# Performance work log

Hardware: AMD Instinct MI355X
Metric: run time of the kernel (lower is better)

## Reference

```python
import jax, jax.numpy as jnp
import numpy as np

EPS = 1e-6
DIM, B, H, W = 64, 8, 256, 256

def _ln2d(x, w, b):
    # LayerNorm over channel dim per spatial location (NAFNet LayerNorm2d)
    mu = x.mean(1, keepdims=True)
    var = ((x - mu) ** 2).mean(1, keepdims=True)
    return (x - mu) * jax.lax.rsqrt(var + EPS) * w[None, :, None, None] + b[None, :, None, None]

def _pw(x, w, b):  # 1x1 conv
    return jnp.einsum('bchw,oc->bohw', x, w) + b[None, :, None, None]

def _dw(x, w, b):  # depthwise conv, SAME padding
    out = jax.lax.conv_general_dilated(x, w, (1, 1), 'SAME',
                                       feature_group_count=x.shape[1],
                                       dimension_numbers=('NCHW', 'OIHW', 'NCHW'))
    return out + b[None, :, None, None]

def _dwt(x, filt):  # haar-style non-overlapping 2x2 DWT; filt [4,2,2]
    Bn, C, Hh, Ww = x.shape
    xr = x.reshape(Bn, C, Hh // 2, 2, Ww // 2, 2)
    s = jnp.einsum('bchpwq,kpq->bkchw', xr, filt)
    return s.reshape(Bn, 4 * C, Hh // 2, Ww // 2)  # [LL..., LH..., HL..., HH...]

def _idwt(s, filt):  # inverse (transpose of orthonormal transform)
    Bn, C4, h, w = s.shape
    C = C4 // 4
    sr = s.reshape(Bn, 4, C, h, w)
    xr = jnp.einsum('bkchw,kpq->bchpwq', sr, filt)
    return xr.reshape(Bn, C, 2 * h, 2 * w)

def setup_inputs() -> dict:
    key = jax.random.key(0)
    ks = jax.random.split(key, 24)
    C = DIM
    f32 = jnp.float32
    rn = lambda k, sh, sc=0.02: (jax.random.normal(k, sh, dtype=f32) * sc)
    haar = jnp.array([[[0.5, 0.5], [0.5, 0.5]],
                      [[-0.5, -0.5], [0.5, 0.5]],
                      [[-0.5, 0.5], [-0.5, 0.5]],
                      [[0.5, -0.5], [-0.5, 0.5]]], dtype=f32)
    return {
        'x_in': jax.random.normal(ks[0], (B, C, H, W), dtype=f32),
        'filt': haar,  # learnable wavelet filters, haar-initialized
        'ln1_w': jnp.ones((C,), f32), 'ln1_b': jnp.zeros((C,), f32),
        'w1': rn(ks[1], (6 * C, 4 * C)), 'b1': rn(ks[2], (6 * C,), 0.01),
        'dw5': rn(ks[3], (6 * C, 1, 5, 5), 0.05), 'bdw5': rn(ks[4], (6 * C,), 0.01),
        'dw3': rn(ks[5], (6 * C, 1, 3, 3), 0.05), 'bdw3': rn(ks[6], (6 * C,), 0.01),
        'w2': rn(ks[7], (4 * C, 6 * C)), 'b2': rn(ks[8], (4 * C,), 0.01),
        'w_sca': rn(ks[9], (C, C)), 'b_sca': rn(ks[10], (C,), 0.01),
        'w3': rn(ks[11], (C, C)), 'b3': rn(ks[12], (C,), 0.01),
        'beta': rn(ks[13], (1, C, 1, 1), 0.1),
        'ln2_w': jnp.ones((C,), f32), 'ln2_b': jnp.zeros((C,), f32),
        'w4': rn(ks[14], (2 * C, C)), 'b4': rn(ks[15], (2 * C,), 0.01),
        'w5': rn(ks[16], (C, C)), 'b5': rn(ks[17], (C,), 0.01),
        'gamma': rn(ks[18], (1, C, 1, 1), 0.1),
    }

def reference(x_in, filt, ln1_w, ln1_b, w1, b1, dw5, bdw5, dw3, bdw3, w2, b2,
              w_sca, b_sca, w3, b3, beta, ln2_w, ln2_b, w4, b4, w5, b5, gamma):
    x = _ln2d(x_in, ln1_w, ln1_b)
    # LWN: DWT -> 1x1 expand -> depthwise(5) -> depthwise(3) -> 1x1 -> IDWT
    s = _dwt(x, filt)                  # [B,4C,H/2,W/2]
    s = _pw(s, w1, b1)                 # [B,6C,.,.]
    s = jax.nn.gelu(_dw(s, dw5, bdw5), approximate=False)
    s = jax.nn.gelu(_dw(s, dw3, bdw3), approximate=False)
    s = _pw(s, w2, b2)                 # [B,4C,.,.]
    x = _idwt(s, filt)                 # [B,C,H,W]
    # simplified channel attention (SCA)
    att = _pw(x.mean((2, 3), keepdims=True), w_sca, b_sca)
    x = x * att
    x = _pw(x, w3, b3)
    y = x_in + x * beta                # dual-residual branch 1
    x = _ln2d(y, ln2_w, ln2_b)
    x = _pw(x, w4, b4)                 # [B,2C,H,W]
    a, g = jnp.split(x, 2, axis=1)
    x = _pw(a * g, w5, b5)             # SimpleGate + project
    return y + x * gamma
```

## Files before the change

### kernel.cpp

```cpp
#include <hip/hip_runtime.h>
#include <math.h>

#define BDIM 8
#define CDIM 64
#define HDIM 256
#define WDIM 256
#define HW  (HDIM*WDIM)
#define HW2 (128*128)
#define C4  256
#define C6  384

typedef __attribute__((ext_vector_type(8))) short short8;
typedef __attribute__((ext_vector_type(4))) float f32x4;

__device__ __forceinline__ ushort f2bf(float x) {
    unsigned u = __float_as_uint(x);
    unsigned r = (u + 0x7fffu + ((u >> 16) & 1u)) >> 16;
    return (ushort)r;
}
__device__ __forceinline__ float bf2f(ushort v) {
    return __uint_as_float(((unsigned)v) << 16);
}
__device__ __forceinline__ float gelu(float x) {
    return 0.5f * x * (1.0f + erff(x * 0.70710678118654752f));
}

__global__ void k_cvt_bf16(const float* __restrict__ src, ushort* __restrict__ dst, int n) {
    int i = blockIdx.x * 256 + threadIdx.x;
    if (i < n) dst[i] = f2bf(src[i]);
}

__global__ __launch_bounds__(256) void k_ln_dwt(
    const float* __restrict__ X, const float* __restrict__ filt,
    const float* __restrict__ lw, const float* __restrict__ lb,
    ushort* __restrict__ S)
{
    const int b   = blockIdx.z;
    const int tid = threadIdx.x;
    const int pb  = tid >> 2;
    const int cg  = tid & 3;
    const int p   = blockIdx.x * 64 + pb;
    const int h2  = p >> 6;
    const int wp  = p & 63;
    float f[16];
#pragma unroll
    for (int i = 0; i < 16; ++i) f[i] = filt[i];

    const float* xb = X + (size_t)b * CDIM * HW + (size_t)(2 * h2) * WDIM + 4 * wp;
    const int c0 = cg * 16;

    float s0 = 0.f, q0 = 0.f, s1 = 0.f, q1 = 0.f;
    for (int c = c0; c < c0 + 16; ++c) {
        const float* pr = xb + (size_t)c * HW;
        float4 r0 = *(const float4*)pr;
        float4 r1 = *(const float4*)(pr + WDIM);
        s0 += r0.x + r0.y + r1.x + r1.y;
        q0 += r0.x*r0.x + r0.y*r0.y + r1.x*r1.x + r1.y*r1.y;
        s1 += r0.z + r0.w + r1.z + r1.w;
        q1 += r0.z*r0.z + r0.w*r0.w + r1.z*r1.z + r1.w*r1.w;
    }
    s0 += __shfl_xor(s0, 1); q0 += __shfl_xor(q0, 1);
    s1 += __shfl_xor(s1, 1); q1 += __shfl_xor(q1, 1);
    s0 += __shfl_xor(s0, 2); q0 += __shfl_xor(q0, 2);
    s1 += __shfl_xor(s1, 2); q1 += __shfl_xor(q1, 2);
    const float inv = 1.0f / 64.0f;
    float m0 = s0 * inv, m1 = s1 * inv;
    float rs0 = rsqrtf(fmaxf(q0 * inv - m0 * m0, 0.f) + 1e-6f);
    float rs1 = rsqrtf(fmaxf(q1 * inv - m1 * m1, 0.f) + 1e-6f);

    const int n = h2 * 128 + 2 * wp;
    ushort* Sp = S + (size_t)b * C4 * HW2;
    for (int c = c0; c < c0 + 16; ++c) {
        const float* pr = xb + (size_t)c * HW;
        float4 r0 = *(const float4*)pr;
        float4 r1 = *(const float4*)(pr + WDIM);
        float wv = lw[c], bv = lb[c];
        float a00 = (r0.x - m0) * rs0 * wv + bv;
        float a01 = (r0.y - m0) * rs0 * wv + bv;
        float a10 = (r1.x - m0) * rs0 * wv + bv;
        float a11 = (r1.y - m0) * rs0 * wv + bv;
        float b00 = (r0.z - m1) * rs1 * wv + bv;
        float b01 = (r0.w - m1) * rs1 * wv + bv;
        float b10 = (r1.z - m1) * rs1 * wv + bv;
        float b11 = (r1.w - m1) * rs1 * wv + bv;
#pragma unroll
        for (int k = 0; k < 4; ++k) {
            float va = f[k*4+0]*a00 + f[k*4+1]*a01 + f[k*4+2]*a10 + f[k*4+3]*a11;
            float vb = f[k*4+0]*b00 + f[k*4+1]*b01 + f[k*4+2]*b10 + f[k*4+3]*b11;
            unsigned pk = (unsigned)f2bf(va) | ((unsigned)f2bf(vb) << 16);
            *(unsigned*)&Sp[(size_t)(k * CDIM + c) * HW2 + n] = pk;
        }
    }
}

template<bool BF16OUT>
__global__ __launch_bounds__(256) void k_pw_mfma(
    const ushort* __restrict__ A, const float* __restrict__ bias,
    const ushort* __restrict__ Xg, void* __restrict__ Yg,
    int M, int K, int N)
{
    const int b  = blockIdx.z;
    const int m0 = blockIdx.y * 128;
    const int n0 = blockIdx.x * 128;
    const ushort* X = Xg + (size_t)b * K * N;

    __shared__ ushort As[128][72];
    __shared__ ushort Bs[128][72];

    const int tid = threadIdx.x;
    const int l   = tid & 63, w = tid >> 6;
    const int wr  = w >> 1, wc = w & 1;
    const int lr  = l & 15, lg = l >> 4;

    const int blr = tid & 15;
    const int bng = tid >> 4;
    const int k0c = blr * 4;
    const int n0t = bng * 8;

    f32x4 acc[4][4];
#pragma unroll
    for (int i = 0; i < 4; ++i)
#pragma unroll
        for (int j = 0; j < 4; ++j) acc[i][j] = (f32x4){0.f, 0.f, 0.f, 0.f};

    for (int k0 = 0; k0 < K; k0 += 64) {
        uint4 av[4], bv[4];
#pragma unroll
        for (int i = 0; i < 4; ++i) {
            int c = tid + 256 * i;
            int m = c & 127, kc = c >> 7;
            av[i] = *(const uint4*)(A + (size_t)(m0 + m) * K + k0 + kc * 8);
        }
#pragma unroll
        for (int dk = 0; dk < 4; ++dk)
            bv[dk] = *(const uint4*)(X + (size_t)(k0 + k0c + dk) * N + n0 + n0t);

        __syncthreads();
#pragma unroll
        for (int i = 0; i < 4; ++i) {
            int c = tid + 256 * i;
            int m = c & 127, kc = c >> 7;
            *(uint4*)&As[m][kc * 8] = av[i];
        }
#pragma unroll
        for (int j = 0; j < 8; ++j) {
            ushort4 wv;
            wv.x = ((const ushort*)&bv[0])[j];
            wv.y = ((const ushort*)&bv[1])[j];
            wv.z = ((const ushort*)&bv[2])[j];
            wv.w = ((const ushort*)&bv[3])[j];
            *(ushort4*)&Bs[n0t + j][k0c] = wv;
        }
        __syncthreads();

#pragma unroll
        for (int ks = 0; ks < 2; ++ks) {
            short8 af[4], bf[4];
#pragma unroll
            for (int mf = 0; mf < 4; ++mf)
                af[mf] = *(const short8*)&As[wr * 64 + mf * 16 + lr][ks * 32 + lg * 8];
#pragma unroll
            for (int nf = 0; nf < 4; ++nf)
                bf[nf] = *(const short8*)&Bs[wc * 64 + nf * 16 + lr][ks * 32 + lg * 8];
#pragma unroll
            for (int mf = 0; mf < 4; ++mf)
#pragma unroll
                for (int nf = 0; nf < 4; ++nf)
                    acc[mf][nf] = __builtin_amdgcn_mfma_f32_16x16x32_bf16(
                        af[mf], bf[nf], acc[mf][nf], 0, 0, 0);
        }
    }

#pragma unroll
    for (int mf = 0; mf < 4; ++mf) {
#pragma unroll
        for (int r = 0; r < 4; ++r) {
            int m = m0 + wr * 64 + mf * 16 + lg * 4 + r;
            float bi = bias[m];
#pragma unroll
            for (int nf = 0; nf < 4; ++nf) {
                int n = n0 + wc * 64 + nf * 16 + lr;
                float v = acc[mf][nf][r] + bi;
                if (BF16OUT)
                    ((ushort*)Yg)[(size_t)b * M * N + (size_t)m * N + n] = f2bf(v);
                else
                    ((float*)Yg)[(size_t)b * M * N + (size_t)m * N + n] = v;
            }
        }
    }
}

__global__ __launch_bounds__(256) void k_dw_fused(
    const ushort* __restrict__ X, const float* __restrict__ W5,
    const float* __restrict__ B5, const float* __restrict__ W3,
    const float* __restrict__ B3, ushort* __restrict__ Y)
{
    const int b = blockIdx.z, ch = blockIdx.y;
    const int ty0 = (blockIdx.x >> 1) * 64, tx0 = (blockIdx.x & 1) * 64;
    __shared__ ushort in_s[70][72];
    __shared__ float  mid_s[66][68];
    const ushort* Xc = X + ((size_t)b * C6 + ch) * HW2;
    ushort* Yc = Y + ((size_t)b * C6 + ch) * HW2;
    const int tid = threadIdx.x;

    float w5[25], w3[9];
#pragma unroll
    for (int i = 0; i < 25; ++i) w5[i] = W5[ch * 25 + i];
#pragma unroll
    for (int i = 0; i < 9; ++i)  w3[i] = W3[ch * 9 + i];
    const float b5v = B5[ch], b3v = B3[ch];

    for (int e = tid; e < 70 * 72; e += 256) {
        int r = e / 72, c = e - r * 72;
        int gy = ty0 + r - 3, gx = tx0 + c - 3;
        ushort v = 0;
        if (c < 70 && (unsigned)gy < 128u && (unsigned)gx < 128u)
            v = Xc[gy * 128 + gx];
        in_s[r][c] = v;
    }
    __syncthreads();

    for (int g = tid; g < 66 * 17; g += 256) {
        int r = g / 17, cg = g - r * 17;
        int c = cg * 4;
        float xin[5][8];
#pragma unroll
        for (int dr = 0; dr < 5; ++dr) {
            ushort4 lo = *(const ushort4*)&in_s[r + dr][c];
            ushort4 hi = *(const ushort4*)&in_s[r + dr][c + 4];
            xin[dr][0] = bf2f(lo.x); xin[dr][1] = bf2f(lo.y);
            xin[dr][2] = bf2f(lo.z); xin[dr][3] = bf2f(lo.w);
            xin[dr][4] = bf2f(hi.x); xin[dr][5] = bf2f(hi.y);
            xin[dr][6] = bf2f(hi.z); xin[dr][7] = bf2f(hi.w);
        }
        int gy = ty0 + r - 1;
        float o[4];
#pragma unroll
        for (int j = 0; j < 4; ++j) {
            float acc = b5v;
#pragma unroll
            for (int dr = 0; dr < 5; ++dr)
#pragma unroll
                for (int dc = 0; dc < 5; ++dc)
                    acc += xin[dr][j + dc] * w5[dr * 5 + dc];
            int gx = tx0 + c + j - 1;
            bool ok = ((unsigned)gy < 128u) && ((unsigned)gx < 128u);
            o[j] = ok ? gelu(acc) : 0.f;
        }
        *(float4*)&mid_s[r][c] = make_float4(o[0], o[1], o[2], o[3]);
    }
    __syncthreads();

    for (int g = tid; g < 64 * 16; g += 256) {
        int r = g >> 4, c = (g & 15) * 4;
        float mv[3][8];
#pragma unroll
        for (int dr = 0; dr < 3; ++dr) {
            float4 a = *(const float4*)&mid_s[r + dr][c];
            float4 bq = *(const float4*)&mid_s[r + dr][c + 4];
            mv[dr][0] = a.x; mv[dr][1] = a.y; mv[dr][2] = a.z; mv[dr][3] = a.w;
            mv[dr][4] = bq.x; mv[dr][5] = bq.y; mv[dr][6] = bq.z; mv[dr][7] = bq.w;
        }
        ushort4 ov;
        float oo[4];
#pragma unroll
        for (int j = 0; j < 4; ++j) {
            float acc = b3v;
#pragma unroll
            for (int dr = 0; dr < 3; ++dr)
#pragma unroll
                for (int dc = 0; dc < 3; ++dc)
                    acc += mv[dr][j + dc] * w3[dr * 3 + dc];
            oo[j] = gelu(acc);
        }
        ov.x = f2bf(oo[0]); ov.y = f2bf(oo[1]); ov.z = f2bf(oo[2]); ov.w = f2bf(oo[3]);
        *(ushort4*)&Yc[(ty0 + r) * 128 + tx0 + c] = ov;
    }
}

__global__ __launch_bounds__(256) void k_idwt(
    const float* __restrict__ S, const float* __restrict__ filt,
    float* __restrict__ Xw, float* __restrict__ sumbuf)
{
    const int b = blockIdx.z, c = blockIdx.y;
    const int tid = threadIdx.x;
    const int n = blockIdx.x * 256 + tid;
    const int h2 = n >> 7, w2 = n & 127;
    float f[16];
#pragma unroll
    for (int i = 0; i < 16; ++i) f[i] = filt[i];
    float sv[4];
#pragma unroll
    for (int k = 0; k < 4; ++k)
        sv[k] = S[((size_t)b * C4 + k * CDIM + c) * HW2 + n];
    float* xp = Xw + ((size_t)b * CDIM + c) * HW + (size_t)(2 * h2) * WDIM + 2 * w2;
    float local = 0.f;
#pragma unroll
    for (int p = 0; p < 2; ++p)
#pragma unroll
        for (int q = 0; q < 2; ++q) {
            float v = sv[0] * f[0*4 + p*2 + q] + sv[1] * f[1*4 + p*2 + q]
                    + sv[2] * f[2*4 + p*2 + q] + sv[3] * f[3*4 + p*2 + q];
            xp[p * WDIM + q] = v;
            local += v;
        }
    __shared__ float red[256];
    red[tid] = local;
    __syncthreads();
    for (int off = 128; off > 0; off >>= 1) {
        if (tid < off) red[tid] += red[tid + off];
        __syncthreads();
    }
    if (tid == 0) atomicAdd(&sumbuf[b * CDIM + c], red[0]);
}

__global__ void k_att(const float* __restrict__ sumbuf, const float* __restrict__ Wsca,
                      const float* __restrict__ bsca, float* __restrict__ att)
{
    int t = threadIdx.x;
    int b = t >> 6, o = t & 63;
    float acc = bsca[o];
    const float s = 1.0f / (float)HW;
    for (int c = 0; c < 64; ++c)
        acc += Wsca[o * 64 + c] * (sumbuf[b * 64 + c] * s);
    att[t] = acc;
}

__global__ __launch_bounds__(256) void k_sca_pw3(
    const float* __restrict__ Xw, const float* __restrict__ Xin,
    const float* __restrict__ att, const float* __restrict__ W3,
    const float* __restrict__ b3, const float* __restrict__ beta,
    float* __restrict__ Yb)
{
    __shared__ __align__(16) float w3s[64 * 64];
    __shared__ float atts[64], b3s[64], bets[64];
    const int tid = threadIdx.x, b = blockIdx.z;
    for (int i = tid; i < 4096; i += 256) w3s[i] = W3[i];
    if (tid < 64) { atts[tid] = att[b * 64 + tid]; b3s[tid] = b3[tid]; bets[tid] = beta[tid]; }
    __syncthreads();
    const size_t n = (size_t)blockIdx.x * 256 + tid;
    const size_t base = (size_t)b * 64 * HW + n;
    float v[64];
#pragma unroll
    for (int c = 0; c < 64; ++c) v[c] = Xw[base + (size_t)c * HW] * atts[c];
    for (int o = 0; o < 64; ++o) {
        float acc = b3s[o];
        const float4* wr = (const float4*)&w3s[o * 64];
#pragma unroll
        for (int c4 = 0; c4 < 16; ++c4) {
            float4 wv = wr[c4]; int c = c4 * 4;
            acc += wv.x*v[c] + wv.y*v[c+1] + wv.z*v[c+2] + wv.w*v[c+3];
        }
        Yb[base + (size_t)o * HW] = Xin[base + (size_t)o * HW] + acc * bets[o];
    }
}

__global__ __launch_bounds__(256) void k_ln2_pw4(
    const float* __restrict__ Yb, const float* __restrict__ lw,
    const float* __restrict__ lb, const float* __restrict__ W4,
    const float* __restrict__ b4, float* __restrict__ Hb)
{
    __shared__ __align__(16) float w4s[128 * 64];
    __shared__ float b4s[128], lws[64], lbs[64];
    const int tid = threadIdx.x, b = blockIdx.z;
    for (int i = tid; i < 8192; i += 256) w4s[i] = W4[i];
    if (tid < 128) b4s[tid] = b4[tid];
    if (tid < 64) { lws[tid] = lw[tid]; lbs[tid] = lb[tid]; }
    __syncthreads();
    const size_t n = (size_t)blockIdx.x * 256 + tid;
    const size_t base = (size_t)b * 64 * HW + n;
    float t[64]; float sum = 0.f, sq = 0.f;
#pragma unroll
    for (int c = 0; c < 64; ++c) {
        float yv = Yb[base + (size_t)c * HW];
        t[c] = yv; sum += yv; sq += yv * yv;
    }
    float mu = sum * (1.0f / 64.0f);
    float var = sq * (1.0f / 64.0f) - mu * mu;
    float rs = rsqrtf(fmaxf(var, 0.f) + 1e-6f);
#pragma unroll
    for (int c = 0; c < 64; ++c) t[c] = (t[c] - mu) * rs * lws[c] + lbs[c];
    for (int j = 0; j < 64; ++j) {
        float aj = b4s[j], gj = b4s[j + 64];
        const float4* wa = (const float4*)&w4s[j * 64];
        const float4* wg = (const float4*)&w4s[(j + 64) * 64];
#pragma unroll
        for (int c4 = 0; c4 < 16; ++c4) {
            float4 va = wa[c4], vg = wg[c4]; int c = c4 * 4;
            aj += va.x*t[c] + va.y*t[c+1] + va.z*t[c+2] + va.w*t[c+3];
            gj += vg.x*t[c] + vg.y*t[c+1] + vg.z*t[c+2] + vg.w*t[c+3];
        }
        Hb[((size_t)b * 64 + j) * HW + n] = aj * gj;
    }
}

__global__ __launch_bounds__(256) void k_pw5_out(
    const float* __restrict__ Yb, const float* __restrict__ Hb,
    const float* __restrict__ W5, const float* __restrict__ b5,
    const float* __restrict__ gamma, float* __restrict__ Out)
{
    __shared__ __align__(16) float w5s[64 * 64];
    __shared__ float b5s[64], gs[64];
    const int tid = threadIdx.x, b = blockIdx.z;
    for (int i = tid; i < 4096; i += 256) w5s[i] = W5[i];
    if (tid < 64) { b5s[tid] = b5[tid]; gs[tid] = gamma[tid]; }
    __syncthreads();
    const size_t n = (size_t)blockIdx.x * 256 + tid;
    const size_t base = (size_t)b * 64 * HW + n;
    float hv[64];
#pragma unroll
    for (int j = 0; j < 64; ++j) hv[j] = Hb[base + (size_t)j * HW];
    for (int o = 0; o < 64; ++o) {
        float acc = b5s[o];
        const float4* wr = (const float4*)&w5s[o * 64];
#pragma unroll
        for (int j4 = 0; j4 < 16; ++j4) {
            float4 wv = wr[j4]; int j = j4 * 4;
            acc += wv.x*hv[j] + wv.y*hv[j+1] + wv.z*hv[j+2] + wv.w*hv[j+3];
        }
        Out[base + (size_t)o * HW] = Yb[base + (size_t)o * HW] + acc * gs[o];
    }
}

extern "C" void kernel_launch(void* const* d_in, const int* in_sizes, int n_in,
                              void* d_out, int out_size, void* d_ws, size_t ws_size,
                              hipStream_t stream) {
    const float* x_in  = (const float*)d_in[0];
    const float* filt  = (const float*)d_in[1];
    const float* ln1_w = (const float*)d_in[2];
    const float* ln1_b = (const float*)d_in[3];
    const float* w1    = (const float*)d_in[4];
    const float* b1    = (const float*)d_in[5];
    const float* dw5   = (const float*)d_in[6];
    const float* bdw5  = (const float*)d_in[7];
    const float* dw3   = (const float*)d_in[8];
    const float* bdw3  = (const float*)d_in[9];
    const float* w2    = (const float*)d_in[10];
    const float* b2    = (const float*)d_in[11];
    const float* w_sca = (const float*)d_in[12];
    const float* b_sca = (const float*)d_in[13];
    const float* w3    = (const float*)d_in[14];
    const float* b3    = (const float*)d_in[15];
    const float* beta  = (const float*)d_in[16];
    const float* ln2_w = (const float*)d_in[17];
    const float* ln2_b = (const float*)d_in[18];
    const float* w4    = (const float*)d_in[19];
    const float* b4    = (const float*)d_in[20];
    const float* w5    = (const float*)d_in[21];
    const float* b5    = (const float*)d_in[22];
    const float* gamma = (const float*)d_in[23];
    float* out = (float*)d_out;

    const size_t PB = (size_t)CDIM * HW * 4;
    int bc = 8;
    while (bc > 1 && 3 * PB * (size_t)bc + 512 * 1024 > ws_size) bc >>= 1;
    const int nchunk = BDIM / bc;

    char* base = (char*)d_ws;
    char* R1 = base;
    char* R2 = base + PB * bc;
    char* R3 = base + 2 * PB * bc;
    ushort* w1b  = (ushort*)(base + 3 * PB * bc);
    ushort* w2b  = w1b + C6 * C4;
    float*  stats = (float*)(w2b + C6 * C4);
    float*  attv  = stats + (size_t)bc * 64;

    k_cvt_bf16<<<(C6 * C4 + 255) / 256, 256, 0, stream>>>(w1, w1b, C6 * C4);
    k_cvt_bf16<<<(C6 * C4 + 255) / 256, 256, 0, stream>>>(w2, w2b, C6 * C4);

    ushort* S   = (ushort*)R1;
    ushort* p1  = (ushort*)R2;
    ushort* d3  = (ushort*)R1;
    float*  p2  = (float*)R2;
    float*  xw  = (float*)R3;
    float*  yb  = (float*)R1;
    float*  hb  = (float*)R2;

    for (int ck = 0; ck < nchunk; ++ck) {
        const float* xin_c = x_in + (size_t)ck * bc * CDIM * HW;
        float* out_c = out + (size_t)ck * bc * CDIM * HW;

        hipMemsetAsync(stats, 0, (size_t)bc * 64 * sizeof(float), stream);

        k_ln_dwt<<<dim3(128, 1, bc), 256, 0, stream>>>(xin_c, filt, ln1_w, ln1_b, S);
        k_pw_mfma<true ><<<dim3(128, 3, bc), 256, 0, stream>>>(w1b, b1, S,  (void*)p1, C6, C4, HW2);
        k_dw_fused<<<dim3(4, C6, bc), 256, 0, stream>>>(p1, dw5, bdw5, dw3, bdw3, d3);
        k_pw_mfma<false><<<dim3(128, 2, bc), 256, 0, stream>>>(w2b, b2, d3, (void*)p2, C4, C6, HW2);
        k_idwt<<<dim3(64, CDIM, bc), 256, 0, stream>>>(p2, filt, xw, stats);
        k_att<<<1, bc * 64, 0, stream>>>(stats, w_sca, b_sca, attv);
        k_sca_pw3<<<dim3(256, 1, bc), 256, 0, stream>>>(xw, xin_c, attv, w3, b3, beta, yb);
        k_ln2_pw4<<<dim3(256, 1, bc), 256, 0, stream>>>(yb, ln2_w, ln2_b, w4, b4, hb);
        k_pw5_out<<<dim3(256, 1, bc), 256, 0, stream>>>(yb, hb, w5, b5, gamma, out_c);
    }
}
```

Baseline: 1.316 ms.

## Fuse LN2/pw4/gate/pw5 tail and store intermediates in bf16

Merges the LN2+pw4+SimpleGate and pw5+residual kernels into a single per-pixel kernel, so the 64-channel gated intermediate is never written to or re-read from global memory. LayerNorm weights are folded into W4 by a small prep kernel, and W5 is transposed so it can be accumulated as outer products. The second MFMA pointwise output and the IDWT output are now stored as bf16 rather than fp32, halving that traffic at the cost of precision. Weights are read directly from global/constant memory instead of being staged in shared memory, and the fused kernel holds many more registers, which may lower occupancy.

After: 1.330 ms. About the same (+1.1%).

```diff
diff --git a/kernel.cpp b/kernel.cpp
--- a/kernel.cpp
+++ b/kernel.cpp
@@ -28,6 +28,30 @@
 __global__ void k_cvt_bf16(const float* __restrict__ src, ushort* __restrict__ dst, int n) {
     int i = blockIdx.x * 256 + threadIdx.x;
     if (i < n) dst[i] = f2bf(src[i]);
+}
+
+__global__ void k_prep(const float* __restrict__ W4, const float* __restrict__ b4,
+                       const float* __restrict__ lw, const float* __restrict__ lb,
+                       const float* __restrict__ W5,
+                       float* __restrict__ W4L, float* __restrict__ KaMa,
+                       float* __restrict__ W5T)
+{
+    int t = threadIdx.x;
+    if (t < 128) {
+        float ka = b4[t], ma = 0.f;
+        for (int c = 0; c < 64; ++c) {
+            float w = W4[t * 64 + c];
+            W4L[t * 64 + c] = w * lw[c];
+            ka += w * lb[c];
+            ma += w * lw[c];
+        }
+        KaMa[t] = ka;
+        KaMa[128 + t] = ma;
+    } else if (t < 192) {
+        int o = t - 128;
+        for (int j = 0; j < 64; ++j)
+            W5T[j * 64 + o] = W5[o * 64 + j];
+    }
 }
 
 __global__ __launch_bounds__(256) void k_ln_dwt(
@@ -279,8 +303,8 @@
 }
 
 __global__ __launch_bounds__(256) void k_idwt(
-    const float* __restrict__ S, const float* __restrict__ filt,
-    float* __restrict__ Xw, float* __restrict__ sumbuf)
+    const ushort* __restrict__ S, const float* __restrict__ filt,
+    ushort* __restrict__ Xw, float* __restrict__ sumbuf)
 {
     const int b = blockIdx.z, c = blockIdx.y;
     const int tid = threadIdx.x;
@@ -292,18 +316,19 @@
     float sv[4];
 #pragma unroll
     for (int k = 0; k < 4; ++k)
-        sv[k] = S[((size_t)b * C4 + k * CDIM + c) * HW2 + n];
-    float* xp = Xw + ((size_t)b * CDIM + c) * HW + (size_t)(2 * h2) * WDIM + 2 * w2;
+        sv[k] = bf2f(S[((size_t)b * C4 + k * CDIM + c) * HW2 + n]);
+    ushort* xp = Xw + ((size_t)b * CDIM + c) * HW + (size_t)(2 * h2) * WDIM + 2 * w2;
     float local = 0.f;
 #pragma unroll
-    for (int p = 0; p < 2; ++p)
-#pragma unroll
-        for (int q = 0; q < 2; ++q) {
-            float v = sv[0] * f[0*4 + p*2 + q] + sv[1] * f[1*4 + p*2 + q]
-                    + sv[2] * f[2*4 + p*2 + q] + sv[3] * f[3*4 + p*2 + q];
-            xp[p * WDIM + q] = v;
-            local += v;
-        }
+    for (int p = 0; p < 2; ++p) {
+        float v0 = sv[0] * f[0*4 + p*2 + 0] + sv[1] * f[1*4 + p*2 + 0]
+                 + sv[2] * f[2*4 + p*2 + 0] + sv[3] * f[3*4 + p*2 + 0];
+        float v1 = sv[0] * f[0*4 + p*2 + 1] + sv[1] * f[1*4 + p*2 + 1]
+                 + sv[2] * f[2*4 + p*2 + 1] + sv[3] * f[3*4 + p*2 + 1];
+        unsigned pk = (unsigned)f2bf(v0) | ((unsigned)f2bf(v1) << 16);
+        *(unsigned*)&xp[p * WDIM] = pk;
+        local += v0 + v1;
+    }
     __shared__ float red[256];
     red[tid] = local;
     __syncthreads();
@@ -327,99 +352,75 @@
 }
 
 __global__ __launch_bounds__(256) void k_sca_pw3(
-    const float* __restrict__ Xw, const float* __restrict__ Xin,
+    const ushort* __restrict__ Xw, const float* __restrict__ Xin,
     const float* __restrict__ att, const float* __restrict__ W3,
     const float* __restrict__ b3, const float* __restrict__ beta,
     float* __restrict__ Yb)
 {
-    __shared__ __align__(16) float w3s[64 * 64];
-    __shared__ float atts[64], b3s[64], bets[64];
     const int tid = threadIdx.x, b = blockIdx.z;
-    for (int i = tid; i < 4096; i += 256) w3s[i] = W3[i];
-    if (tid < 64) { atts[tid] = att[b * 64 + tid]; b3s[tid] = b3[tid]; bets[tid] = beta[tid]; }
-    __syncthreads();
     const size_t n = (size_t)blockIdx.x * 256 + tid;
     const size_t base = (size_t)b * 64 * HW + n;
+    const float* attb = att + b * 64;
     float v[64];
 #pragma unroll
-    for (int c = 0; c < 64; ++c) v[c] = Xw[base + (size_t)c * HW] * atts[c];
+    for (int c = 0; c < 64; ++c)
+        v[c] = bf2f(Xw[base + (size_t)c * HW]) * attb[c];
     for (int o = 0; o < 64; ++o) {
-        float acc = b3s[o];
-        const float4* wr = (const float4*)&w3s[o * 64];
-#pragma unroll
-        for (int c4 = 0; c4 < 16; ++c4) {
-            float4 wv = wr[c4]; int c = c4 * 4;
-            acc += wv.x*v[c] + wv.y*v[c+1] + wv.z*v[c+2] + wv.w*v[c+3];
-        }
-        Yb[base + (size_t)o * HW] = Xin[base + (size_t)o * HW] + acc * bets[o];
-    }
-}
-
-__global__ __launch_bounds__(256) void k_ln2_pw4(
-    const float* __restrict__ Yb, const float* __restrict__ lw,
-    const float* __restrict__ lb, const float* __restrict__ W4,
-    const float* __restrict__ b4, float* __restrict__ Hb)
-{
-    __shared__ __align__(16) float w4s[128 * 64];
-    __shared__ float b4s[128], lws[64], lbs[64];
+        const float* w = W3 + o * 64;
+        float a0 = 0.f, a1 = 0.f, a2 = 0.f, a3 = 0.f;
+#pragma unroll
+        for (int c = 0; c < 64; c += 4) {
+            a0 += w[c]   * v[c];   a1 += w[c+1] * v[c+1];
+            a2 += w[c+2] * v[c+2]; a3 += w[c+3] * v[c+3];
+        }
+        Yb[base + (size_t)o * HW] = Xin[base + (size_t)o * HW]
+                                  + (((a0 + a1) + (a2 + a3)) + b3[o]) * beta[o];
+    }
+}
+
+__global__ __launch_bounds__(256) void k_tail2(
+    const float* __restrict__ Yb, const float* __restrict__ W4L,
+    const float* __restrict__ KaMa, const float* __restrict__ W5T,
+    const float* __restrict__ b5, const float* __restrict__ gamma,
+    float* __restrict__ Out)
+{
     const int tid = threadIdx.x, b = blockIdx.z;
-    for (int i = tid; i < 8192; i += 256) w4s[i] = W4[i];
-    if (tid < 128) b4s[tid] = b4[tid];
-    if (tid < 64) { lws[tid] = lw[tid]; lbs[tid] = lb[tid]; }
-    __syncthreads();
     const size_t n = (size_t)blockIdx.x * 256 + tid;
     const size_t base = (size_t)b * 64 * HW + n;
-    float t[64]; float sum = 0.f, sq = 0.f;
+    float y[64];
+    float s = 0.f, q = 0.f;
 #pragma unroll
     for (int c = 0; c < 64; ++c) {
         float yv = Yb[base + (size_t)c * HW];
-        t[c] = yv; sum += yv; sq += yv * yv;
-    }
-    float mu = sum * (1.0f / 64.0f);
-    float var = sq * (1.0f / 64.0f) - mu * mu;
-    float rs = rsqrtf(fmaxf(var, 0.f) + 1e-6f);
-#pragma unroll
-    for (int c = 0; c < 64; ++c) t[c] = (t[c] - mu) * rs * lws[c] + lbs[c];
+        y[c] = yv; s += yv; q += yv * yv;
+    }
+    const float mu = s * (1.0f / 64.0f);
+    const float var = q * (1.0f / 64.0f) - mu * mu;
+    const float rs = rsqrtf(fmaxf(var, 0.f) + 1e-6f);
+    float acc[64];
+#pragma unroll
+    for (int o = 0; o < 64; ++o) acc[o] = b5[o];
     for (int j = 0; j < 64; ++j) {
-        float aj = b4s[j], gj = b4s[j + 64];
-        const float4* wa = (const float4*)&w4s[j * 64];
-        const float4* wg = (const float4*)&w4s[(j + 64) * 64];
-#pragma unroll
-        for (int c4 = 0; c4 < 16; ++c4) {
-            float4 va = wa[c4], vg = wg[c4]; int c = c4 * 4;
-            aj += va.x*t[c] + va.y*t[c+1] + va.z*t[c+2] + va.w*t[c+3];
-            gj += vg.x*t[c] + vg.y*t[c+1] + vg.z*t[c+2] + vg.w*t[c+3];
-        }
-        Hb[((size_t)b * 64 + j) * HW + n] = aj * gj;
-    }
-}
-
-__global__ __launch_bounds__(256) void k_pw5_out(
-    const float* __restrict__ Yb, const float* __restrict__ Hb,
-    const float* __restrict__ W5, const float* __restrict__ b5,
-    const float* __restrict__ gamma, float* __restrict__ Out)
-{
-    __shared__ __align__(16) float w5s[64 * 64];
-    __shared__ float b5s[64], gs[64];
-    const int tid = threadIdx.x, b = blockIdx.z;
-    for (int i = tid; i < 4096; i += 256) w5s[i] = W5[i];
-    if (tid < 64) { b5s[tid] = b5[tid]; gs[tid] = gamma[tid]; }
-    __syncthreads();
-    const size_t n = (size_t)blockIdx.x * 256 + tid;
-    const size_t base = (size_t)b * 64 * HW + n;
-    float hv[64];
-#pragma unroll
-    for (int j = 0; j < 64; ++j) hv[j] = Hb[base + (size_t)j * HW];
-    for (int o = 0; o < 64; ++o) {
-        float acc = b5s[o];
-        const float4* wr = (const float4*)&w5s[o * 64];
-#pragma unroll
-        for (int j4 = 0; j4 < 16; ++j4) {
-            float4 wv = wr[j4]; int j = j4 * 4;
-            acc += wv.x*hv[j] + wv.y*hv[j+1] + wv.z*hv[j+2] + wv.w*hv[j+3];
-        }
-        Out[base + (size_t)o * HW] = Yb[base + (size_t)o * HW] + acc * gs[o];
-    }
+        const float* wa = W4L + j * 64;
+        const float* wg = W4L + (j + 64) * 64;
+        float a0=0.f,a1=0.f,a2=0.f,a3=0.f,g0=0.f,g1=0.f,g2=0.f,g3=0.f;
+#pragma unroll
+        for (int c = 0; c < 64; c += 4) {
+            a0 += wa[c]   * y[c];   a1 += wa[c+1] * y[c+1];
+            a2 += wa[c+2] * y[c+2]; a3 += wa[c+3] * y[c+3];
+            g0 += wg[c]   * y[c];   g1 += wg[c+1] * y[c+1];
+            g2 += wg[c+2] * y[c+2]; g3 += wg[c+3] * y[c+3];
+        }
+        float aj = rs * (((a0 + a1) + (a2 + a3)) - mu * KaMa[128 + j]) + KaMa[j];
+        float gj = rs * (((g0 + g1) + (g2 + g3)) - mu * KaMa[192 + j]) + KaMa[64 + j];
+        float hj = aj * gj;
+        const float* w5r = W5T + j * 64;
+#pragma unroll
+        for (int o = 0; o < 64; ++o) acc[o] += w5r[o] * hj;
+    }
+#pragma unroll
+    for (int o = 0; o < 64; ++o)
+        Out[base + (size_t)o * HW] = y[o] + acc[o] * gamma[o];
 }
 
 extern "C" void kernel_launch(void* const* d_in, const int* in_sizes, int n_in,
@@ -462,19 +463,22 @@
     char* R3 = base + 2 * PB * bc;
     ushort* w1b  = (ushort*)(base + 3 * PB * bc);
     ushort* w2b  = w1b + C6 * C4;
-    float*  stats = (float*)(w2b + C6 * C4);
+    float*  w4l  = (float*)(w2b + C6 * C4);
+    float*  kama = w4l + 128 * 64;
+    float*  w5t  = kama + 256;
+    float*  stats = w5t + 64 * 64;
     float*  attv  = stats + (size_t)bc * 64;
 
     k_cvt_bf16<<<(C6 * C4 + 255) / 256, 256, 0, stream>>>(w1, w1b, C6 * C4);
     k_cvt_bf16<<<(C6 * C4 + 255) / 256, 256, 0, stream>>>(w2, w2b, C6 * C4);
+    k_prep<<<1, 256, 0, stream>>>(w4, b4, ln2_w, ln2_b, w5, w4l, kama, w5t);
 
     ushort* S   = (ushort*)R1;
     ushort* p1  = (ushort*)R2;
     ushort* d3  = (ushort*)R1;
-    float*  p2  = (float*)R2;
-    float*  xw  = (float*)R3;
+    ushort* p2  = (ushort*)R2;
+    ushort* xw  = (ushort*)R3;
     float*  yb  = (float*)R1;
-    float*  hb  = (float*)R2;
 
     for (int ck = 0; ck < nchunk; ++ck) {
         const float* xin_c = x_in + (size_t)ck * bc * CDIM * HW;
@@ -483,13 +487,12 @@
         hipMemsetAsync(stats, 0, (size_t)bc * 64 * sizeof(float), stream);
 
         k_ln_dwt<<<dim3(128, 1, bc), 256, 0, stream>>>(xin_c, filt, ln1_w, ln1_b, S);
-        k_pw_mfma<true ><<<dim3(128, 3, bc), 256, 0, stream>>>(w1b, b1, S,  (void*)p1, C6, C4, HW2);
+        k_pw_mfma<true><<<dim3(128, 3, bc), 256, 0, stream>>>(w1b, b1, S,  (void*)p1, C6, C4, HW2);
         k_dw_fused<<<dim3(4, C6, bc), 256, 0, stream>>>(p1, dw5, bdw5, dw3, bdw3, d3);
-        k_pw_mfma<false><<<dim3(128, 2, bc), 256, 0, stream>>>(w2b, b2, d3, (void*)p2, C4, C6, HW2);
+        k_pw_mfma<true><<<dim3(128, 2, bc), 256, 0, stream>>>(w2b, b2, d3, (void*)p2, C4, C6, HW2);
         k_idwt<<<dim3(64, CDIM, bc), 256, 0, stream>>>(p2, filt, xw, stats);
         k_att<<<1, bc * 64, 0, stream>>>(stats, w_sca, b_sca, attv);
         k_sca_pw3<<<dim3(256, 1, bc), 256, 0, stream>>>(xw, xin_c, attv, w3, b3, beta, yb);
-        k_ln2_pw4<<<dim3(256, 1, bc), 256, 0, stream>>>(yb, ln2_w, ln2_b, w4, b4, hb);
-        k_pw5_out<<<dim3(256, 1, bc), 256, 0, stream>>>(yb, hb, w5, b5, gamma, out_c);
-    }
-}
+        k_tail2<<<dim3(256, 1, bc), 256, 0, stream>>>(yb, w4l, kama, w5t, b5, gamma, out_c);
+    }
+}
```
